# Optimization experiments

Measured on AMD Instinct MI355X. Metric: run time of the kernel, lower is better.

## Reference

```python
import jax, jax.numpy as jnp
import numpy as np

N_NODES = 50000
N_EDGES = 800000
IN_DIM = 96
HID_DIM = 96


def setup_inputs() -> dict:
    key = jax.random.key(0)
    ks = jax.random.split(key, 8)
    inputs = jax.random.normal(ks[0], (N_NODES, IN_DIM), dtype=jnp.float32)
    factor = jax.random.uniform(ks[1], (N_EDGES, 1), dtype=jnp.float32)
    src = jax.random.randint(ks[2], (N_EDGES,), 0, N_NODES, dtype=jnp.int32)
    dst = jax.random.randint(ks[3], (N_EDGES,), 0, N_NODES, dtype=jnp.int32)
    # Linear params (torch nn.Linear: y = x @ W.T + b), uniform(-1/sqrt(fan_in), ..)
    s1 = 1.0 / np.sqrt(IN_DIM)
    s2 = 1.0 / np.sqrt(HID_DIM)
    W1 = jax.random.uniform(ks[4], (HID_DIM, IN_DIM), minval=-s1, maxval=s1, dtype=jnp.float32)
    b1 = jax.random.uniform(ks[5], (HID_DIM,), minval=-s1, maxval=s1, dtype=jnp.float32)
    W2 = jax.random.uniform(ks[6], (IN_DIM, HID_DIM), minval=-s2, maxval=s2, dtype=jnp.float32)
    b2 = jax.random.uniform(ks[7], (IN_DIM,), minval=-s2, maxval=s2, dtype=jnp.float32)
    return {"inputs": inputs, "W1": W1, "b1": b1, "W2": W2, "b2": b2,
            "factor": factor, "src": src, "dst": dst}


def _propagate(feat, factor, src, dst, n_nodes):
    # message = h[src] * edge_factor ; reduce = sum at dst
    msg = feat[src] * factor                       # [E, D]
    return jax.ops.segment_sum(msg, dst, num_segments=n_nodes)


def reference(inputs, W1, b1, W2, b2, factor, src, dst):
    n = inputs.shape[0]
    # in-degree norm: deg^{-1/2}, clamped at 1
    deg = jax.ops.segment_sum(jnp.ones((src.shape[0],), inputs.dtype), dst,
                              num_segments=n)
    norm = jnp.maximum(deg, 1.0) ** -0.5           # [N]
    norm = norm[:, None]                           # [N, 1]

    feat = (inputs @ W1.T + b1) * norm             # [N, H]
    h = jnp.tanh(_propagate(feat, factor, src, dst, n))

    feat = (h @ W2.T + b2) * norm                  # [N, D]
    h = jnp.tanh(_propagate(feat, factor, src, dst, n))

    # dgl.mean_nodes over a single graph -> [1, D]; unsqueeze(-1) -> [1, D, 1]
    pooled = jnp.mean(h, axis=0, keepdims=True)[..., None]
    return jnp.tanh(pooled)
```

## Files before the change

kernel.cpp:

```cpp
#include <hip/hip_runtime.h>
#include <math.h>
#include <type_traits>

#define N_NODES 50000
#define N_EDGES 800000
#define DIM 96
#define BCH 12
#define SCAN_BLK 256
#define NBLK ((N_NODES + SCAN_BLK - 1) / SCAN_BLK)
#define GBLK 512
#define NPB 42
#define NBG ((N_NODES + NPB - 1) / NPB)
#define CAP 768
#define R1_ROWS 24
#define R1_BLOCKS ((NBG + R1_ROWS - 1) / R1_ROWS)
#define SC_PASSES 4
#define SC_WIN ((N_NODES + SC_PASSES - 1) / SC_PASSES)
#define F8_SCALE 16.0f
#define F8_INV   0.0625f

typedef short v8s __attribute__((ext_vector_type(8)));
typedef float v4f __attribute__((ext_vector_type(4)));
typedef float v2f __attribute__((ext_vector_type(2)));

__device__ __forceinline__ unsigned short f2bf(float f) {
    unsigned int u = __float_as_uint(f);
    u += 0x7FFFu + ((u >> 16) & 1u);
    return (unsigned short)(u >> 16);
}
__device__ __forceinline__ unsigned int pack2bf(float lo, float hi) {
    return (unsigned int)f2bf(lo) | ((unsigned int)f2bf(hi) << 16);
}

__device__ __forceinline__ float fast_tanh(float x) {
    float ax = fabsf(x);
    float t = __expf(-2.0f * ax);
    float r = (1.0f - t) / (1.0f + t);
    return copysignf(r, x);
}

__device__ __forceinline__ void accf8(float* a, uint2 v, float f) {
    v2f p0 = __builtin_amdgcn_cvt_pk_f32_fp8(v.x, false);
    v2f p1 = __builtin_amdgcn_cvt_pk_f32_fp8(v.x, true);
    v2f p2 = __builtin_amdgcn_cvt_pk_f32_fp8(v.y, false);
    v2f p3 = __builtin_amdgcn_cvt_pk_f32_fp8(v.y, true);
    a[0] += p0.x * f; a[1] += p0.y * f;
    a[2] += p1.x * f; a[3] += p1.y * f;
    a[4] += p2.x * f; a[5] += p2.y * f;
    a[6] += p3.x * f; a[7] += p3.y * f;
}

union U4S8 { uint4 u; v8s s; };


__global__ void count_deg(const int* __restrict__ dst, int* __restrict__ deg,
                          int* __restrict__ rank) {
    int e = blockIdx.x * blockDim.x + threadIdx.x;
    if (e < N_EDGES) rank[e] = atomicAdd(&deg[dst[e]], 1);
}

__global__ void deg_partials(const int* __restrict__ deg, float* __restrict__ norm,
                             int* __restrict__ partials) {
    int b = blockIdx.x, t = threadIdx.x;
    int n = b * SCAN_BLK + t;
    int v = 0;
    if (n < N_NODES) {
        v = deg[n];
        norm[n] = rsqrtf(fmaxf((float)v, 1.0f));
    }
    int s = v;
#pragma unroll
    for (int off = 32; off > 0; off >>= 1) s += __shfl_down(s, off, 64);
    __shared__ int ws_[4];
    if ((t & 63) == 0) ws_[t >> 6] = s;
    __syncthreads();
    if (t == 0) partials[b] = ws_[0] + ws_[1] + ws_[2] + ws_[3];
}

__global__ void scan_partials(const int* __restrict__ partials, int* __restrict__ pprefix) {
    __shared__ int sm[SCAN_BLK];
    int t = threadIdx.x;
    int v = (t < NBLK) ? partials[t] : 0;
    sm[t] = v;
    __syncthreads();
    for (int off = 1; off < SCAN_BLK; off <<= 1) {
        int u = (t >= off) ? sm[t - off] : 0;
        __syncthreads();
        sm[t] += u;
        __syncthreads();
    }
    if (t < NBLK) pprefix[t] = sm[t] - v;
}

__global__ void make_offsets(const int* __restrict__ deg, const int* __restrict__ pprefix,
                             int* __restrict__ offs) {
    __shared__ int sm[SCAN_BLK];
    int b = blockIdx.x, t = threadIdx.x;
    int idx = b * SCAN_BLK + t;
    int v = (idx < N_NODES) ? deg[idx] : 0;
    sm[t] = v;
    __syncthreads();
    for (int off = 1; off < SCAN_BLK; off <<= 1) {
        int u = (t >= off) ? sm[t - off] : 0;
        __syncthreads();
        sm[t] += u;
        __syncthreads();
    }
    if (idx < N_NODES) offs[idx] = pprefix[b] + sm[t] - v;
    if (b == 0 && t == 0) offs[N_NODES] = N_EDGES;
}

__global__ void scatter_edges(const int* __restrict__ src, const int* __restrict__ dst,
                              const float* __restrict__ factor, const int* __restrict__ rank,
                              const int* __restrict__ offs, int2* __restrict__ entries) {
    int tid0 = blockIdx.x * blockDim.x + threadIdx.x;
    int stride = gridDim.x * blockDim.x;
#pragma unroll 1
    for (int pass = 0; pass < SC_PASSES; ++pass) {
        int lo = pass * SC_WIN;
        int hi = min(lo + SC_WIN, N_NODES);
#pragma unroll 1
        for (int e = tid0; e < N_EDGES; e += stride) {
            int d = dst[e];
            if (d >= lo && d < hi) {
                int pos = offs[d] + rank[e];
                entries[pos] = make_int2(src[e], __float_as_int(factor[e]));
            }
        }
    }
}


__global__ void swizzle_W(const float* __restrict__ W, uint4* __restrict__ bsw) {
    int idx = blockIdx.x * blockDim.x + threadIdx.x;
    if (idx >= 18 * 64) return;
    int t = idx >> 6, lane = idx & 63;
    int kt = t / 6, jt = t % 6;
    int quad = lane >> 4, l16 = lane & 15;
    const float4* wp = (const float4*)(W + (size_t)(jt * 16 + l16) * DIM + kt * 32 + quad * 8);
    float4 w0 = wp[0], w1 = wp[1];
    bsw[idx] = make_uint4(pack2bf(w0.x, w0.y), pack2bf(w0.z, w0.w),
                          pack2bf(w1.x, w1.y), pack2bf(w1.z, w1.w));
}


template <typename T>
__global__ __launch_bounds__(256) void gemm_mfma(const T* __restrict__ X,
                                                 const uint4* __restrict__ bsw,
                                                 const float* __restrict__ bias,
                                                 const float* __restrict__ norm,
                                                 unsigned char* __restrict__ out) {
    int tid = threadIdx.x;
    int wave = tid >> 6, lane = tid & 63;
    int quad = lane >> 4, l16 = lane & 15;
    int n0 = blockIdx.x * 64 + wave * 16;
    int node = n0 + l16;
    int rowc = min(node, N_NODES - 1);

    uint4 bfr[18];
#pragma unroll
    for (int t = 0; t < 18; ++t) bfr[t] = bsw[t * 64 + lane];

    v4f acc[6];
#pragma unroll
    for (int jt = 0; jt < 6; ++jt) acc[jt] = (v4f)(0.0f);

#pragma unroll
    for (int kt = 0; kt < 3; ++kt) {
        U4S8 x;
        if constexpr (std::is_same_v<T, float>) {
            const float4* xp = (const float4*)(X + (size_t)rowc * DIM + kt * 32 + quad * 8);
            float4 x0 = xp[0], x1 = xp[1];
            x.u = make_uint4(pack2bf(x0.x, x0.y), pack2bf(x0.z, x0.w),
                             pack2bf(x1.x, x1.y), pack2bf(x1.z, x1.w));
        } else {
            x.u = *(const uint4*)(X + (size_t)rowc * DIM + kt * 32 + quad * 8);
        }
#pragma unroll
        for (int jt = 0; jt < 6; ++jt) {
            U4S8 w; w.u = bfr[kt * 6 + jt];
            acc[jt] = __builtin_amdgcn_mfma_f32_16x16x32_bf16(w.s, x.s, acc[jt], 0, 0, 0);
        }
    }

    if (node < N_NODES) {
        float nm = norm[node] * F8_SCALE;
#pragma unroll
        for (int jt = 0; jt < 6; ++jt) {
            float4 bj = *(const float4*)(bias + jt * 16 + quad * 4);
            float v0 = (acc[jt][0] + bj.x) * nm;
            float v1 = (acc[jt][1] + bj.y) * nm;
            float v2 = (acc[jt][2] + bj.z) * nm;
            float v3 = (acc[jt][3] + bj.w) * nm;
            unsigned int w = (unsigned int)__builtin_amdgcn_cvt_pk_fp8_f32(v0, v1, 0, false);
            w = (unsigned int)__builtin_amdgcn_cvt_pk_fp8_f32(v2, v3, (int)w, true);
            *(unsigned int*)(out + (size_t)node * DIM + jt * 16 + quad * 4) = w;
        }
    }
}


template <bool POOL>
__global__ __launch_bounds__(GBLK) void gather_agg_f8(
        const unsigned char* __restrict__ feat,
        const int* __restrict__ offs,
        const int2* __restrict__ entries,
        unsigned short* __restrict__ out,
        float* __restrict__ partials) {
    __shared__ int2 ents[CAP];
    __shared__ float pool[DIM];
    __shared__ int sh_base, sh_cnt;
    int tid = threadIdx.x;
    int n0 = blockIdx.x * NPB;
    int n1 = min(n0 + NPB, N_NODES);
    if (POOL && tid < DIM) pool[tid] = 0.f;
    if (tid == 0) { sh_base = offs[n0]; sh_cnt = offs[n1] - sh_base; }
    __syncthreads();
    int base = sh_base, cnt = sh_cnt;

    int nl = tid / BCH;
    int c  = tid - nl * BCH;
    int n  = n0 + nl;
    bool active = (tid < NPB * BCH) && (n < N_NODES);
    int lb = 0, le = 0;
    if (active) { lb = offs[n] - base; le = offs[n + 1] - base; }

    float a0[8], a1[8];
#pragma unroll
    for (int i = 0; i < 8; ++i) { a0[i] = 0.f; a1[i] = 0.f; }

    for (int tb = 0; tb < cnt; tb += CAP) {
        int tcnt = min(cnt - tb, CAP);
        if (tb) __syncthreads();
        for (int i = tid; i < tcnt; i += GBLK) ents[i] = entries[base + tb + i];
        __syncthreads();
        int s = max(lb - tb, 0), e = min(le - tb, tcnt);
        int p = s;
        for (; p + 7 < e; p += 8) {
            int2 q0 = ents[p + 0], q1 = ents[p + 1], q2 = ents[p + 2], q3 = ents[p + 3];
            int2 q4 = ents[p + 4], q5 = ents[p + 5], q6 = ents[p + 6], q7 = ents[p + 7];
            uint2 v0 = *((const uint2*)(feat + (size_t)q0.x * DIM) + c);
            uint2 v1 = *((const uint2*)(feat + (size_t)q1.x * DIM) + c);
            uint2 v2 = *((const uint2*)(feat + (size_t)q2.x * DIM) + c);
            uint2 v3 = *((const uint2*)(feat + (size_t)q3.x * DIM) + c);
            uint2 v4 = *((const uint2*)(feat + (size_t)q4.x * DIM) + c);
            uint2 v5 = *((const uint2*)(feat + (size_t)q5.x * DIM) + c);
            uint2 v6 = *((const uint2*)(feat + (size_t)q6.x * DIM) + c);
            uint2 v7 = *((const uint2*)(feat + (size_t)q7.x * DIM) + c);
            accf8(a0, v0, __int_as_float(q0.y));
            accf8(a1, v1, __int_as_float(q1.y));
            accf8(a0, v2, __int_as_float(q2.y));
            accf8(a1, v3, __int_as_float(q3.y));
            accf8(a0, v4, __int_as_float(q4.y));
            accf8(a1, v5, __int_as_float(q5.y));
            accf8(a0, v6, __int_as_float(q6.y));
            accf8(a1, v7, __int_as_float(q7.y));
        }
        for (; p + 3 < e; p += 4) {
            int2 q0 = ents[p], q1 = ents[p + 1], q2 = ents[p + 2], q3 = ents[p + 3];
            uint2 v0 = *((const uint2*)(feat + (size_t)q0.x * DIM) + c);
            uint2 v1 = *((const uint2*)(feat + (size_t)q1.x * DIM) + c);
            uint2 v2 = *((const uint2*)(feat + (size_t)q2.x * DIM) + c);
            uint2 v3 = *((const uint2*)(feat + (size_t)q3.x * DIM) + c);
            accf8(a0, v0, __int_as_float(q0.y));
            accf8(a1, v1, __int_as_float(q1.y));
            accf8(a0, v2, __int_as_float(q2.y));
            accf8(a1, v3, __int_as_float(q3.y));
        }
        for (; p < e; ++p) {
            int2 q0 = ents[p];
            uint2 v0 = *((const uint2*)(feat + (size_t)q0.x * DIM) + c);
            accf8(a0, v0, __int_as_float(q0.y));
        }
    }

#pragma unroll
    for (int i = 0; i < 8; ++i) a0[i] = fast_tanh((a0[i] + a1[i]) * F8_INV);
    if (!POOL) {
        if (active) {
            uint4 o;
            o.x = pack2bf(a0[0], a0[1]);
            o.y = pack2bf(a0[2], a0[3]);
            o.z = pack2bf(a0[4], a0[5]);
            o.w = pack2bf(a0[6], a0[7]);
            ((uint4*)out)[n * BCH + c] = o;
        }
    } else {
        if (active) {
#pragma unroll
            for (int i = 0; i < 8; ++i) atomicAdd(&pool[c * 8 + i], a0[i]);
        }
        __syncthreads();
        if (tid < DIM) partials[(size_t)blockIdx.x * DIM + tid] = pool[tid];
    }
}


__global__ void reduce_stage1(const float* __restrict__ poolpart, float* __restrict__ stage1) {
    __shared__ float pool[DIM];
    int b = blockIdx.x, t = threadIdx.x;
    if (t < DIM) pool[t] = 0.f;
    __syncthreads();
    const int base = b * R1_ROWS * DIM;
    float loc = 0.f;
    int lastc = -1;
    for (int i = t; i < R1_ROWS * DIM; i += 256) {
        int gi = base + i;
        if (gi < NBG * DIM) {
            int col = i % DIM;
            if (col != lastc) {
                if (lastc >= 0) atomicAdd(&pool[lastc], loc);
                lastc = col; loc = 0.f;
            }
            loc += poolpart[gi];
        }
    }
    if (lastc >= 0) atomicAdd(&pool[lastc], loc);
    __syncthreads();
    if (t < DIM) stage1[b * DIM + t] = pool[t];
}

__global__ void reduce_stage2(const float* __restrict__ stage1, float* __restrict__ out) {
    __shared__ float sm[960];
    int t = threadIdx.x;
    int col = t % DIM, slice = t / DIM;
    float s = 0.f;
    for (int k = slice; k < R1_BLOCKS; k += 10) s += stage1[k * DIM + col];
    sm[t] = s;
    __syncthreads();
    if (t < DIM) {
        float tot = 0.f;
#pragma unroll
        for (int i = 0; i < 10; ++i) tot += sm[i * DIM + t];
        out[t] = tanhf(tot * (1.0f / N_NODES));
    }
}


extern "C" void kernel_launch(void* const* d_in, const int* in_sizes, int n_in,
                              void* d_out, int out_size, void* d_ws, size_t ws_size,
                              hipStream_t stream) {
    const float* inputs = (const float*)d_in[0];
    const float* W1     = (const float*)d_in[1];
    const float* b1     = (const float*)d_in[2];
    const float* W2     = (const float*)d_in[3];
    const float* b2     = (const float*)d_in[4];
    const float* factor = (const float*)d_in[5];
    const int*   src    = (const int*)d_in[6];
    const int*   dst    = (const int*)d_in[7];
    float* out = (float*)d_out;

    char* ws = (char*)d_ws;
    int*            deg      = (int*)(ws + 0);
    int*            rank     = (int*)(ws + 262144);
    int*            offs     = (int*)(ws + 3670016);
    float*          norm     = (float*)(ws + 3932160);
    int*            partials = (int*)(ws + 4194304);
    int*            pprefix  = (int*)(ws + 4196352);
    int2*           entries  = (int2*)(ws + 4456448);
    unsigned char*  bufA     = (unsigned char*)(ws + 11534336);
    unsigned short* bufB     = (unsigned short*)(ws + 16777216);
    float*          poolpart = (float*)(ws + 26738688);
    float*          stage1   = (float*)(ws + 27787264);
    uint4*          bsw1     = (uint4*)(ws + 27836416);
    uint4*          bsw2     = (uint4*)(ws + 27856896);

    swizzle_W<<<5, 256, 0, stream>>>(W1, bsw1);
    swizzle_W<<<5, 256, 0, stream>>>(W2, bsw2);

    hipMemsetAsync(deg, 0, N_NODES * sizeof(int), stream);
    count_deg<<<(N_EDGES + 255) / 256, 256, 0, stream>>>(dst, deg, rank);
    deg_partials<<<NBLK, SCAN_BLK, 0, stream>>>(deg, norm, partials);
    scan_partials<<<1, SCAN_BLK, 0, stream>>>(partials, pprefix);
    make_offsets<<<NBLK, SCAN_BLK, 0, stream>>>(deg, pprefix, offs);
    scatter_edges<<<2048, 256, 0, stream>>>(src, dst, factor, rank, offs, entries);

    const int GEMM_BLOCKS = (N_NODES + 63) / 64;

    gemm_mfma<float><<<GEMM_BLOCKS, 256, 0, stream>>>(inputs, bsw1, b1, norm, bufA);
    gather_agg_f8<false><<<NBG, GBLK, 0, stream>>>(bufA, offs, entries, bufB, nullptr);

    gemm_mfma<unsigned short><<<GEMM_BLOCKS, 256, 0, stream>>>(bufB, bsw2, b2, norm, bufA);
    gather_agg_f8<true><<<NBG, GBLK, 0, stream>>>(bufA, offs, entries, nullptr, poolpart);

    reduce_stage1<<<R1_BLOCKS, 256, 0, stream>>>(poolpart, stage1);
    reduce_stage2<<<1, 960, 0, stream>>>(stage1, out);
}
```

Measured before the change: 231.9 us.

## Fuse second-layer GEMM into first gather epilogue via LDS tile

```diff
diff --git a/kernel.cpp b/kernel.cpp
--- a/kernel.cpp
+++ b/kernel.cpp
@@ -18,6 +18,7 @@
 #define SC_WIN ((N_NODES + SC_PASSES - 1) / SC_PASSES)
 #define F8_SCALE 16.0f
 #define F8_INV   0.0625f
+#define TILE_SH 104
 
 typedef short v8s __attribute__((ext_vector_type(8)));
 typedef float v4f __attribute__((ext_vector_type(4)));
@@ -200,20 +201,21 @@
 }
 
 
-template <bool POOL>
-__global__ __launch_bounds__(GBLK) void gather_agg_f8(
+__global__ __launch_bounds__(GBLK) void gather_fuse(
         const unsigned char* __restrict__ feat,
         const int* __restrict__ offs,
         const int2* __restrict__ entries,
-        unsigned short* __restrict__ out,
-        float* __restrict__ partials) {
+        const uint4* __restrict__ bsw2,
+        const float* __restrict__ bias2,
+        const float* __restrict__ norm,
+        unsigned char* __restrict__ feat2) {
     __shared__ int2 ents[CAP];
-    __shared__ float pool[DIM];
+    __shared__ __align__(16) unsigned short h1s[48 * TILE_SH];
     __shared__ int sh_base, sh_cnt;
     int tid = threadIdx.x;
+    for (int i = tid; i < 48 * TILE_SH / 2; i += GBLK) ((unsigned int*)h1s)[i] = 0u;
     int n0 = blockIdx.x * NPB;
     int n1 = min(n0 + NPB, N_NODES);
-    if (POOL && tid < DIM) pool[tid] = 0.f;
     if (tid == 0) { sh_base = offs[n0]; sh_cnt = offs[n1] - sh_base; }
     __syncthreads();
     int base = sh_base, cnt = sh_cnt;
@@ -274,25 +276,137 @@
         }
     }
 
+    if (active) {
+#pragma unroll
+        for (int i = 0; i < 8; ++i) a0[i] = fast_tanh((a0[i] + a1[i]) * F8_INV);
+        uint4 o;
+        o.x = pack2bf(a0[0], a0[1]);
+        o.y = pack2bf(a0[2], a0[3]);
+        o.z = pack2bf(a0[4], a0[5]);
+        o.w = pack2bf(a0[6], a0[7]);
+        *(uint4*)&h1s[nl * TILE_SH + c * 8] = o;
+    }
+    __syncthreads();
+
+    int wave = tid >> 6, lane = tid & 63;
+    if (wave < 3) {
+        int quad = lane >> 4, l16 = lane & 15;
+        uint4 bfr[18];
+#pragma unroll
+        for (int t = 0; t < 18; ++t) bfr[t] = bsw2[t * 64 + lane];
+        v4f acc[6];
+#pragma unroll
+        for (int jt = 0; jt < 6; ++jt) acc[jt] = (v4f)(0.0f);
+#pragma unroll
+        for (int kt = 0; kt < 3; ++kt) {
+            U4S8 x;
+            x.u = *(const uint4*)&h1s[(wave * 16 + l16) * TILE_SH + kt * 32 + quad * 8];
+#pragma unroll
+            for (int jt = 0; jt < 6; ++jt) {
+                U4S8 w; w.u = bfr[kt * 6 + jt];
+                acc[jt] = __builtin_amdgcn_mfma_f32_16x16x32_bf16(w.s, x.s, acc[jt], 0, 0, 0);
+            }
+        }
+        int local = wave * 16 + l16;
+        int node = n0 + local;
+        if (local < n1 - n0) {
+            float nm = norm[node] * F8_SCALE;
+#pragma unroll
+            for (int jt = 0; jt < 6; ++jt) {
+                float4 bj = *(const float4*)(bias2 + jt * 16 + quad * 4);
+                float v0 = (acc[jt][0] + bj.x) * nm;
+                float v1 = (acc[jt][1] + bj.y) * nm;
+                float v2 = (acc[jt][2] + bj.z) * nm;
+                float v3 = (acc[jt][3] + bj.w) * nm;
+                unsigned int w = (unsigned int)__builtin_amdgcn_cvt_pk_fp8_f32(v0, v1, 0, false);
+                w = (unsigned int)__builtin_amdgcn_cvt_pk_fp8_f32(v2, v3, (int)w, true);
+                *(unsigned int*)(feat2 + (size_t)node * DIM + jt * 16 + quad * 4) = w;
+            }
+        }
+    }
+}
+
+
+__global__ __launch_bounds__(GBLK) void gather_pool(
+        const unsigned char* __restrict__ feat,
+        const int* __restrict__ offs,
+        const int2* __restrict__ entries,
+        float* __restrict__ partials) {
+    __shared__ int2 ents[CAP];
+    __shared__ float pool[DIM];
+    __shared__ int sh_base, sh_cnt;
+    int tid = threadIdx.x;
+    int n0 = blockIdx.x * NPB;
+    int n1 = min(n0 + NPB, N_NODES);
+    if (tid < DIM) pool[tid] = 0.f;
+    if (tid == 0) { sh_base = offs[n0]; sh_cnt = offs[n1] - sh_base; }
+    __syncthreads();
+    int base = sh_base, cnt = sh_cnt;
+
+    int nl = tid / BCH;
+    int c  = tid - nl * BCH;
+    int n  = n0 + nl;
+    bool active = (tid < NPB * BCH) && (n < N_NODES);
+    int lb = 0, le = 0;
+    if (active) { lb = offs[n] - base; le = offs[n + 1] - base; }
+
+    float a0[8], a1[8];
+#pragma unroll
+    for (int i = 0; i < 8; ++i) { a0[i] = 0.f; a1[i] = 0.f; }
+
+    for (int tb = 0; tb < cnt; tb += CAP) {
+        int tcnt = min(cnt - tb, CAP);
+        if (tb) __syncthreads();
+        for (int i = tid; i < tcnt; i += GBLK) ents[i] = entries[base + tb + i];
+        __syncthreads();
+        int s = max(lb - tb, 0), e = min(le - tb, tcnt);
+        int p = s;
+        for (; p + 7 < e; p += 8) {
+            int2 q0 = ents[p + 0], q1 = ents[p + 1], q2 = ents[p + 2], q3 = ents[p + 3];
+            int2 q4 = ents[p + 4], q5 = ents[p + 5], q6 = ents[p + 6], q7 = ents[p + 7];
+            uint2 v0 = *((const uint2*)(feat + (size_t)q0.x * DIM) + c);
+            uint2 v1 = *((const uint2*)(feat + (size_t)q1.x * DIM) + c);
+            uint2 v2 = *((const uint2*)(feat + (size_t)q2.x * DIM) + c);
+            uint2 v3 = *((const uint2*)(feat + (size_t)q3.x * DIM) + c);
+            uint2 v4 = *((const uint2*)(feat + (size_t)q4.x * DIM) + c);
+            uint2 v5 = *((const uint2*)(feat + (size_t)q5.x * DIM) + c);
+            uint2 v6 = *((const uint2*)(feat + (size_t)q6.x * DIM) + c);
+            uint2 v7 = *((const uint2*)(feat + (size_t)q7.x * DIM) + c);
+            accf8(a0, v0, __int_as_float(q0.y));
+            accf8(a1, v1, __int_as_float(q1.y));
+            accf8(a0, v2, __int_as_float(q2.y));
+            accf8(a1, v3, __int_as_float(q3.y));
+            accf8(a0, v4, __int_as_float(q4.y));
+            accf8(a1, v5, __int_as_float(q5.y));
+            accf8(a0, v6, __int_as_float(q6.y));
+            accf8(a1, v7, __int_as_float(q7.y));
+        }
+        for (; p + 3 < e; p += 4) {
+            int2 q0 = ents[p], q1 = ents[p + 1], q2 = ents[p + 2], q3 = ents[p + 3];
+            uint2 v0 = *((const uint2*)(feat + (size_t)q0.x * DIM) + c);
+            uint2 v1 = *((const uint2*)(feat + (size_t)q1.x * DIM) + c);
+            uint2 v2 = *((const uint2*)(feat + (size_t)q2.x * DIM) + c);
+            uint2 v3 = *((const uint2*)(feat + (size_t)q3.x * DIM) + c);
+            accf8(a0, v0, __int_as_float(q0.y));
+            accf8(a1, v1, __int_as_float(q1.y));
+            accf8(a0, v2, __int_as_float(q2.y));
+            accf8(a1, v3, __int_as_float(q3.y));
+        }
+        for (; p < e; ++p) {
+            int2 q0 = ents[p];
+            uint2 v0 = *((const uint2*)(feat + (size_t)q0.x * DIM) + c);
+            accf8(a0, v0, __int_as_float(q0.y));
+        }
+    }
+
 #pragma unroll
     for (int i = 0; i < 8; ++i) a0[i] = fast_tanh((a0[i] + a1[i]) * F8_INV);
-    if (!POOL) {
-        if (active) {
-            uint4 o;
-            o.x = pack2bf(a0[0], a0[1]);
-            o.y = pack2bf(a0[2], a0[3]);
-            o.z = pack2bf(a0[4], a0[5]);
-            o.w = pack2bf(a0[6], a0[7]);
-            ((uint4*)out)[n * BCH + c] = o;
-        }
-    } else {
-        if (active) {
-#pragma unroll
-            for (int i = 0; i < 8; ++i) atomicAdd(&pool[c * 8 + i], a0[i]);
-        }
-        __syncthreads();
-        if (tid < DIM) partials[(size_t)blockIdx.x * DIM + tid] = pool[tid];
-    }
+    if (active) {
+#pragma unroll
+        for (int i = 0; i < 8; ++i) atomicAdd(&pool[c * 8 + i], a0[i]);
+    }
+    __syncthreads();
+    if (tid < DIM) partials[(size_t)blockIdx.x * DIM + tid] = pool[tid];
 }
 
 
@@ -359,7 +473,7 @@
     int*            pprefix  = (int*)(ws + 4196352);
     int2*           entries  = (int2*)(ws + 4456448);
     unsigned char*  bufA     = (unsigned char*)(ws + 11534336);
-    unsigned short* bufB     = (unsigned short*)(ws + 16777216);
+    unsigned char*  bufB     = (unsigned char*)(ws + 16777216);
     float*          poolpart = (float*)(ws + 26738688);
     float*          stage1   = (float*)(ws + 27787264);
     uint4*          bsw1     = (uint4*)(ws + 27836416);
@@ -378,10 +492,10 @@
     const int GEMM_BLOCKS = (N_NODES + 63) / 64;
 
     gemm_mfma<float><<<GEMM_BLOCKS, 256, 0, stream>>>(inputs, bsw1, b1, norm, bufA);
-    gather_agg_f8<false><<<NBG, GBLK, 0, stream>>>(bufA, offs, entries, bufB, nullptr);
-
-    gemm_mfma<unsigned short><<<GEMM_BLOCKS, 256, 0, stream>>>(bufB, bsw2, b2, norm, bufA);
-    gather_agg_f8<true><<<NBG, GBLK, 0, stream>>>(bufA, offs, entries, nullptr, poolpart);
+
+    gather_fuse<<<NBG, GBLK, 0, stream>>>(bufA, offs, entries, bsw2, b2, norm, bufB);
+
+    gather_pool<<<NBG, GBLK, 0, stream>>>(bufB, offs, entries, poolpart);
 
     reduce_stage1<<<R1_BLOCKS, 256, 0, stream>>>(poolpart, stage1);
     reduce_stage2<<<1, 960, 0, stream>>>(stage1, out);
```

Result: faster. 224.2 us (-3.4%).
